# Performance work log

Hardware: AMD Instinct MI355X
Metric: run time of the kernel (lower is better)

The kernel has to match this reference:

```python
import jax, jax.numpy as jnp
import numpy as np

MODEL_DIM = 1024
TOTAL_DIM = 1024
N_HEADS = 16
HEAD_DIM = TOTAL_DIM // N_HEADS


def setup_inputs() -> dict:
    key = jax.random.key(0)
    k1, k2, k3 = jax.random.split(key, 3)
    query = jax.random.normal(k1, (2, 2048, MODEL_DIM), dtype=jnp.float32)
    # nn.Linear(model_dim, 3*total_dim, bias=False): store as [in, out] for x @ W
    W_in = jax.random.normal(k2, (MODEL_DIM, 3 * TOTAL_DIM), dtype=jnp.float32) / np.sqrt(MODEL_DIM)
    W_out = jax.random.normal(k3, (TOTAL_DIM, MODEL_DIM), dtype=jnp.float32) / np.sqrt(TOTAL_DIM)
    return {"query": query, "W_in": W_in, "W_out": W_out}


def reference(query, W_in, W_out):
    B, S, _ = query.shape
    qkv = query @ W_in                      # [B, S, 3*D]
    q, k, v = jnp.split(qkv, 3, axis=-1)    # each [B, S, D]

    def to_heads(t):
        return t.reshape(B, S, N_HEADS, HEAD_DIM).transpose(0, 2, 1, 3)  # [B,H,S,d]

    q, k, v = to_heads(q), to_heads(k), to_heads(v)
    scale = 1.0 / np.sqrt(HEAD_DIM).astype(np.float32)
    scores = jnp.einsum('bhqd,bhkd->bhqk', q, k) * scale  # [B,H,S,S]
    causal = jnp.tril(jnp.ones((S, S), dtype=bool))
    scores = jnp.where(causal, scores, jnp.finfo(scores.dtype).min)
    probs = jax.nn.softmax(scores, axis=-1)
    attn = jnp.einsum('bhqk,bhkd->bhqd', probs, v)        # [B,H,S,d]
    attn = attn.transpose(0, 2, 1, 3).reshape(B, S, TOTAL_DIM)
    return attn @ W_out                     # [B, S, model_dim]
```

## Files before the change

kernel.cpp:

```cpp
#include <hip/hip_runtime.h>


typedef __bf16 bf16x8 __attribute__((ext_vector_type(8)));
typedef float f32x4 __attribute__((ext_vector_type(4)));
typedef int i32x4 __attribute__((ext_vector_type(4)));

#define B_   2
#define S_   2048
#define DM   1024
#define NH   16
#define HD   64
#define N3   3072
#define M_   4096

#define SCALE_LOG2E 0.180336884f

__device__ __forceinline__ unsigned short f2bf(float f) {
  unsigned int u = __float_as_uint(f);
  u += 0x7fffu + ((u >> 16) & 1u);
  return (unsigned short)(u >> 16);
}

__device__ __forceinline__ void gload_lds16(void* lds, const void* g) {
  __builtin_amdgcn_global_load_lds(
      (__attribute__((address_space(1))) void*)g,
      (__attribute__((address_space(3))) void*)lds, 16, 0, 0);
}

__global__ __launch_bounds__(256) void f32_to_bf16_vec(
    const float4* __restrict__ in, unsigned short* __restrict__ out, int n4) {
  int i = blockIdx.x * 256 + threadIdx.x;
  if (i < n4) {
    float4 v = in[i];
    ushort4 o;
    o.x = f2bf(v.x); o.y = f2bf(v.y); o.z = f2bf(v.z); o.w = f2bf(v.w);
    *(ushort4*)(&out[(size_t)i * 4]) = o;
  }
}

__global__ __launch_bounds__(256) void transpose_f32_bf16(
    const float* __restrict__ in, unsigned short* __restrict__ out, int R, int C) {
  __shared__ float tile[32][33];
  const int tx = threadIdx.x, ty = threadIdx.y;
  const int x = blockIdx.x * 32 + tx;
  const int y0 = blockIdx.y * 32;
#pragma unroll
  for (int j = 0; j < 32; j += 8)
    tile[ty + j][tx] = in[(size_t)(y0 + ty + j) * C + x];
  __syncthreads();
  const int ox = y0 + tx;
  const int oy0 = blockIdx.x * 32;
#pragma unroll
  for (int j = 0; j < 32; j += 8)
    out[(size_t)(oy0 + ty + j) * R + ox] = f2bf(tile[tx][ty + j]);
}

__global__ __launch_bounds__(256) void transpose_v(
    const unsigned short* __restrict__ qkv, unsigned short* __restrict__ vT) {
  __shared__ unsigned short tile[32][33];
  const int tx = threadIdx.x, ty = threadIdx.y;
  const int c0 = blockIdx.x * 32;
  const int r0 = blockIdx.y * 32;
#pragma unroll
  for (int j = 0; j < 32; j += 8)
    tile[ty + j][tx] = qkv[(size_t)(r0 + ty + j) * N3 + 2 * DM + c0 + tx];
  __syncthreads();
  const int b = r0 >> 11;
  const int srow = (r0 & 2047);
  const int head = c0 >> 6;
#pragma unroll
  for (int j = 0; j < 32; j += 8) {
    const int d = (c0 & 63) + ty + j;
    vT[(size_t)((b * NH + head) * HD + d) * S_ + srow + tx] = tile[tx][ty + j];
  }
}

template <int OUT_BF16>
__global__ __launch_bounds__(256) void gemm_abt(
    const unsigned short* __restrict__ A, const unsigned short* __restrict__ Bt,
    void* __restrict__ Cv, int M, int N, int K) {
  __shared__ __align__(16) unsigned short a_sm[128 * 32];
  __shared__ __align__(16) unsigned short b_sm[128 * 32];
  const int tid = threadIdx.x;
  const int lane = tid & 63, wave = tid >> 6;
  const int quad = lane >> 4, l15 = lane & 15;
  const int row0 = blockIdx.y * 128, col0 = blockIdx.x * 128;
  const int wm = (wave >> 1) * 64, wn = (wave & 1) * 64;

  f32x4 acc[4][4];
#pragma unroll
  for (int i = 0; i < 4; i++)
#pragma unroll
    for (int j = 0; j < 4; j++) acc[i][j] = (f32x4){0.f, 0.f, 0.f, 0.f};

  const int e0 = tid * 8;

  for (int k0 = 0; k0 < K; k0 += 32) {
    __syncthreads();
#pragma unroll
    for (int i = 0; i < 2; i++) {
      int e = e0 + i * 2048;
      int r = e >> 5, c = e & 31;
      gload_lds16(&a_sm[e], &A[(size_t)(row0 + r) * K + k0 + c]);
      gload_lds16(&b_sm[e], &Bt[(size_t)(col0 + r) * K + k0 + c]);
    }
    __syncthreads();

    bf16x8 af[4], bfb[4];
#pragma unroll
    for (int i = 0; i < 4; i++) {
      af[i]  = *(const bf16x8*)&a_sm[(wm + i * 16 + l15) * 32 + quad * 8];
      bfb[i] = *(const bf16x8*)&b_sm[(wn + i * 16 + l15) * 32 + quad * 8];
    }
#pragma unroll
    for (int i = 0; i < 4; i++)
#pragma unroll
      for (int j = 0; j < 4; j++)
        acc[i][j] = __builtin_amdgcn_mfma_f32_16x16x32_bf16(af[i], bfb[j], acc[i][j], 0, 0, 0);
  }

#pragma unroll
  for (int i = 0; i < 4; i++) {
#pragma unroll
    for (int j = 0; j < 4; j++) {
#pragma unroll
      for (int r = 0; r < 4; r++) {
        const int row = row0 + wm + i * 16 + quad * 4 + r;
        const int col = col0 + wn + j * 16 + l15;
        const float v = acc[i][j][r];
        if (OUT_BF16)
          ((unsigned short*)Cv)[(size_t)row * N + col] = f2bf(v);
        else
          ((float*)Cv)[(size_t)row * N + col] = v;
      }
    }
  }
}

__global__ __launch_bounds__(512, 4) void attn_fused3(
    const unsigned short* __restrict__ qkv,
    const unsigned short* __restrict__ vT,
    unsigned short* __restrict__ attnout) {
  const int h = blockIdx.y, b = blockIdx.z;
  const int qt = (b == 0) ? blockIdx.x : (15 - blockIdx.x);
  const int tid = threadIdx.x;
  const int lane = tid & 63, wave = tid >> 6;
  const int quad = lane >> 4, l15 = lane & 15;
  const int sw = l15 & 7;

  __shared__ __align__(16) unsigned short k_sm[2 * 4096];
  __shared__ __align__(16) unsigned short vt_sm[2 * 4096];

  const int Q0 = qt * 128;
  const int qrow = Q0 + wave * 16 + l15;
  const int wrow0 = Q0 + wave * 16;

  bf16x8 qf[2];
  {
    const unsigned short* qp = qkv + (size_t)(b * S_ + qrow) * N3 + h * HD + quad * 8;
    qf[0] = *(const bf16x8*)qp;
    qf[1] = *(const bf16x8*)(qp + 32);
  }

  f32x4 o[4];
#pragma unroll
  for (int n = 0; n < 4; n++) o[n] = (f32x4){0.f, 0.f, 0.f, 0.f};
  float lsum = 0.f;

  const int r0s = tid >> 3;
  const int gch = ((tid & 7) ^ (r0s & 7)) * 8;
  const unsigned short* kgb = qkv + (size_t)(b * S_ + r0s) * N3 + DM + h * HD + gch;
  const unsigned short* vgb = vT + (size_t)((b * NH + h) * HD + r0s) * S_ + gch;

  const int addrA = (((quad * 2) & 3) * 16 + l15) * 4;
  const int addrB = (((quad * 2 + 1) & 3) * 16 + l15) * 4;

  const int nt = 2 * qt + 2;
  gload_lds16(&k_sm[tid * 8], kgb);
  gload_lds16(&vt_sm[tid * 8], vgb);

  for (int t = 0; t < nt; t++) {
    __syncthreads();
    if (t + 1 < nt) {
      const int nb = ((t + 1) & 1) * 4096;
      gload_lds16(&k_sm[nb + tid * 8], kgb + (size_t)(t + 1) * 64 * N3);
      gload_lds16(&vt_sm[nb + tid * 8], vgb + (t + 1) * 64);
    }
    if (t * 64 > wrow0 + 15) continue;

    const unsigned short* kb = &k_sm[(t & 1) * 4096];
    const unsigned short* vb = &vt_sm[(t & 1) * 4096];

    f32x4 s[4];
#pragma unroll
    for (int mb = 0; mb < 4; mb++) s[mb] = (f32x4){0.f, 0.f, 0.f, 0.f};
#pragma unroll
    for (int mb = 0; mb < 4; mb++) {
      const int ro = (mb * 16 + l15) * 64;
      bf16x8 kf0 = *(const bf16x8*)&kb[ro + ((quad ^ sw) << 3)];
      bf16x8 kf1 = *(const bf16x8*)&kb[ro + (((4 + quad) ^ sw) << 3)];
      s[mb] = __builtin_amdgcn_mfma_f32_16x16x32_bf16(kf0, qf[0], s[mb], 0, 0, 0);
      s[mb] = __builtin_amdgcn_mfma_f32_16x16x32_bf16(kf1, qf[1], s[mb], 0, 0, 0);
    }

    if (t * 64 + 63 <= wrow0) {
#pragma unroll
      for (int mb = 0; mb < 4; mb++)
#pragma unroll
        for (int r = 0; r < 4; r++)
          s[mb][r] = exp2f(s[mb][r] * SCALE_LOG2E);
    } else {
      const int kb0 = t * 64 + quad * 4;
#pragma unroll
      for (int mb = 0; mb < 4; mb++)
#pragma unroll
        for (int r = 0; r < 4; r++) {
          const float e = exp2f(s[mb][r] * SCALE_LOG2E);
          s[mb][r] = (kb0 + mb * 16 + r <= qrow) ? e : 0.f;
        }
    }
#pragma unroll
    for (int mb = 0; mb < 4; mb++)
      lsum += (s[mb][0] + s[mb][1]) + (s[mb][2] + s[mb][3]);

    int pk[4][2];
#pragma unroll
    for (int mb = 0; mb < 4; mb++) {
      const unsigned u0 = __float_as_uint(s[mb][0]) + 0x8000u;
      const unsigned u1 = __float_as_uint(s[mb][1]) + 0x8000u;
      const unsigned u2 = __float_as_uint(s[mb][2]) + 0x8000u;
      const unsigned u3 = __float_as_uint(s[mb][3]) + 0x8000u;
      pk[mb][0] = (int)__builtin_amdgcn_perm(u1, u0, 0x07060302u);
      pk[mb][1] = (int)__builtin_amdgcn_perm(u3, u2, 0x07060302u);
    }

    const bool hi = quad >= 2;
#pragma unroll
    for (int ks = 0; ks < 2; ks++) {
      const int m0 = 2 * ks, m1 = m0 + 1;
      const int f0a = __builtin_amdgcn_ds_bpermute(addrA, pk[m0][0]);
      const int f0b = __builtin_amdgcn_ds_bpermute(addrA, pk[m1][0]);
      const int f1a = __builtin_amdgcn_ds_bpermute(addrA, pk[m0][1]);
      const int f1b = __builtin_amdgcn_ds_bpermute(addrA, pk[m1][1]);
      const int f2a = __builtin_amdgcn_ds_bpermute(addrB, pk[m0][0]);
      const int f2b = __builtin_amdgcn_ds_bpermute(addrB, pk[m1][0]);
      const int f3a = __builtin_amdgcn_ds_bpermute(addrB, pk[m0][1]);
      const int f3b = __builtin_amdgcn_ds_bpermute(addrB, pk[m1][1]);
      i32x4 fr;
      fr.x = hi ? f0b : f0a;
      fr.y = hi ? f1b : f1a;
      fr.z = hi ? f2b : f2a;
      fr.w = hi ? f3b : f3a;
      const bf16x8 pfrag = __builtin_bit_cast(bf16x8, fr);
#pragma unroll
      for (int mb = 0; mb < 4; mb++) {
        const int ro = (mb * 16 + l15) * 64;
        bf16x8 vf = *(const bf16x8*)&vb[ro + (((ks * 4 + quad) ^ sw) << 3)];
        o[mb] = __builtin_amdgcn_mfma_f32_16x16x32_bf16(vf, pfrag, o[mb], 0, 0, 0);
      }
    }
  }

  float l = lsum;
  l += __shfl_xor(l, 16);
  l += __shfl_xor(l, 32);
  const float inv = 1.0f / l;
  const size_t grow = (size_t)(b * S_ + qrow);
#pragma unroll
  for (int mb = 0; mb < 4; mb++) {
    ushort4 w;
    w.x = f2bf(o[mb][0] * inv);
    w.y = f2bf(o[mb][1] * inv);
    w.z = f2bf(o[mb][2] * inv);
    w.w = f2bf(o[mb][3] * inv);
    *(ushort4*)&attnout[grow * DM + h * HD + mb * 16 + quad * 4] = w;
  }
}

extern "C" void kernel_launch(void* const* d_in, const int* in_sizes, int n_in,
                              void* d_out, int out_size, void* d_ws, size_t ws_size,
                              hipStream_t stream) {
  const float* query = (const float*)d_in[0];
  const float* w_in  = (const float*)d_in[1];
  const float* w_out = (const float*)d_in[2];
  float* out = (float*)d_out;

  char* ws = (char*)d_ws;
  unsigned short* qbf     = (unsigned short*)(ws);
  unsigned short* vT      = (unsigned short*)(ws);
  unsigned short* w_in_t  = (unsigned short*)(ws + 8388608);
  unsigned short* w_out_t = (unsigned short*)(ws + 14680064);
  unsigned short* qkv     = (unsigned short*)(ws + 16777216);
  unsigned short* attn    = (unsigned short*)(ws + 41943040);

  f32_to_bf16_vec<<<dim3(M_ * DM / 1024), dim3(256), 0, stream>>>(
      (const float4*)query, qbf, M_ * DM / 4);
  transpose_f32_bf16<<<dim3(N3 / 32, DM / 32), dim3(32, 8), 0, stream>>>(w_in, w_in_t, DM, N3);
  transpose_f32_bf16<<<dim3(DM / 32, DM / 32), dim3(32, 8), 0, stream>>>(w_out, w_out_t, DM, DM);
  gemm_abt<1><<<dim3(N3 / 128, M_ / 128), dim3(256), 0, stream>>>(qbf, w_in_t, qkv, M_, N3, DM);
  transpose_v<<<dim3(DM / 32, M_ / 32), dim3(32, 8), 0, stream>>>(qkv, vT);
  attn_fused3<<<dim3(S_ / 128, NH, B_), dim3(512), 0, stream>>>(qkv, vT, attn);
  gemm_abt<0><<<dim3(DM / 128, M_ / 128), dim3(256), 0, stream>>>(attn, w_out_t, out, M_, DM, DM);
}
```

Measured before the change: 203.6 us.

## Fold softmax scale into W_in and give each wave two query row groups

The softmax scale times log2(e) is now folded into the Q columns of the transposed W_in, which removes a multiply per score in the attention kernel. The attention kernel moves from 8 waves of 16 rows each to 4 waves, each covering two 16-row query groups 64 rows apart. K and V fragments are loaded from LDS into registers once per tile and reused for both groups, which halves LDS fragment traffic per MFMA. The cost is higher register pressure, fewer waves per block, and Q rounded to bf16 after scaling, which changes numerics slightly.

```diff
diff --git a/kernel.cpp b/kernel.cpp
--- a/kernel.cpp
+++ b/kernel.cpp
@@ -39,7 +39,8 @@
 }
 
 __global__ __launch_bounds__(256) void transpose_f32_bf16(
-    const float* __restrict__ in, unsigned short* __restrict__ out, int R, int C) {
+    const float* __restrict__ in, unsigned short* __restrict__ out, int R, int C,
+    int scale_rows, float scale) {
   __shared__ float tile[32][33];
   const int tx = threadIdx.x, ty = threadIdx.y;
   const int x = blockIdx.x * 32 + tx;
@@ -51,8 +52,12 @@
   const int ox = y0 + tx;
   const int oy0 = blockIdx.x * 32;
 #pragma unroll
-  for (int j = 0; j < 32; j += 8)
-    out[(size_t)(oy0 + ty + j) * R + ox] = f2bf(tile[tx][ty + j]);
+  for (int j = 0; j < 32; j += 8) {
+    const int orow = oy0 + ty + j;
+    float v = tile[tx][ty + j];
+    if (orow < scale_rows) v *= scale;
+    out[(size_t)orow * R + ox] = f2bf(v);
+  }
 }
 
 __global__ __launch_bounds__(256) void transpose_v(
@@ -137,7 +142,7 @@
   }
 }
 
-__global__ __launch_bounds__(512, 4) void attn_fused3(
+__global__ __launch_bounds__(256, 2) void attn_fused5(
     const unsigned short* __restrict__ qkv,
     const unsigned short* __restrict__ vT,
     unsigned short* __restrict__ attnout) {
@@ -151,21 +156,26 @@
   __shared__ __align__(16) unsigned short k_sm[2 * 4096];
   __shared__ __align__(16) unsigned short vt_sm[2 * 4096];
 
-  const int Q0 = qt * 128;
-  const int qrow = Q0 + wave * 16 + l15;
-  const int wrow0 = Q0 + wave * 16;
-
-  bf16x8 qf[2];
+  const int wrow0 = qt * 128 + wave * 16;
+  const int qrow0 = wrow0 + l15;
+  const int qrow1 = qrow0 + 64;
+
+  bf16x8 qf[2][2];
   {
-    const unsigned short* qp = qkv + (size_t)(b * S_ + qrow) * N3 + h * HD + quad * 8;
-    qf[0] = *(const bf16x8*)qp;
-    qf[1] = *(const bf16x8*)(qp + 32);
-  }
-
-  f32x4 o[4];
-#pragma unroll
-  for (int n = 0; n < 4; n++) o[n] = (f32x4){0.f, 0.f, 0.f, 0.f};
-  float lsum = 0.f;
+    const unsigned short* qp0 = qkv + (size_t)(b * S_ + qrow0) * N3 + h * HD + quad * 8;
+    qf[0][0] = *(const bf16x8*)qp0;
+    qf[0][1] = *(const bf16x8*)(qp0 + 32);
+    const unsigned short* qp1 = qp0 + (size_t)64 * N3;
+    qf[1][0] = *(const bf16x8*)qp1;
+    qf[1][1] = *(const bf16x8*)(qp1 + 32);
+  }
+
+  f32x4 o[2][4];
+#pragma unroll
+  for (int g = 0; g < 2; g++)
+#pragma unroll
+    for (int n = 0; n < 4; n++) o[g][n] = (f32x4){0.f, 0.f, 0.f, 0.f};
+  float lsum[2] = {0.f, 0.f};
 
   const int r0s = tid >> 3;
   const int gch = ((tid & 7) ^ (r0s & 7)) * 8;
@@ -177,103 +187,130 @@
 
   const int nt = 2 * qt + 2;
   gload_lds16(&k_sm[tid * 8], kgb);
+  gload_lds16(&k_sm[tid * 8 + 2048], kgb + (size_t)32 * N3);
   gload_lds16(&vt_sm[tid * 8], vgb);
+  gload_lds16(&vt_sm[tid * 8 + 2048], vgb + (size_t)32 * S_);
 
   for (int t = 0; t < nt; t++) {
     __syncthreads();
     if (t + 1 < nt) {
       const int nb = ((t + 1) & 1) * 4096;
-      gload_lds16(&k_sm[nb + tid * 8], kgb + (size_t)(t + 1) * 64 * N3);
-      gload_lds16(&vt_sm[nb + tid * 8], vgb + (t + 1) * 64);
-    }
-    if (t * 64 > wrow0 + 15) continue;
+      const unsigned short* kgt = kgb + (size_t)(t + 1) * 64 * N3;
+      const unsigned short* vgt = vgb + (t + 1) * 64;
+      gload_lds16(&k_sm[nb + tid * 8], kgt);
+      gload_lds16(&k_sm[nb + tid * 8 + 2048], kgt + (size_t)32 * N3);
+      gload_lds16(&vt_sm[nb + tid * 8], vgt);
+      gload_lds16(&vt_sm[nb + tid * 8 + 2048], vgt + (size_t)32 * S_);
+    }
 
     const unsigned short* kb = &k_sm[(t & 1) * 4096];
     const unsigned short* vb = &vt_sm[(t & 1) * 4096];
-
-    f32x4 s[4];
-#pragma unroll
-    for (int mb = 0; mb < 4; mb++) s[mb] = (f32x4){0.f, 0.f, 0.f, 0.f};
+    const unsigned short* kb0 = kb + l15 * 64 + ((quad ^ sw) << 3);
+    const unsigned short* kb1 = kb + l15 * 64 + (((4 + quad) ^ sw) << 3);
+    const unsigned short* vb0 = vb + l15 * 64 + ((quad ^ sw) << 3);
+    const unsigned short* vb1 = vb + l15 * 64 + (((4 + quad) ^ sw) << 3);
+
+    bf16x8 kf0[4], kf1[4];
 #pragma unroll
     for (int mb = 0; mb < 4; mb++) {
-      const int ro = (mb * 16 + l15) * 64;
-      bf16x8 kf0 = *(const bf16x8*)&kb[ro + ((quad ^ sw) << 3)];
-      bf16x8 kf1 = *(const bf16x8*)&kb[ro + (((4 + quad) ^ sw) << 3)];
-      s[mb] = __builtin_amdgcn_mfma_f32_16x16x32_bf16(kf0, qf[0], s[mb], 0, 0, 0);
-      s[mb] = __builtin_amdgcn_mfma_f32_16x16x32_bf16(kf1, qf[1], s[mb], 0, 0, 0);
-    }
-
-    if (t * 64 + 63 <= wrow0) {
+      kf0[mb] = *(const bf16x8*)&kb0[mb * 1024];
+      kf1[mb] = *(const bf16x8*)&kb1[mb * 1024];
+    }
+    bf16x8 vf0[4], vf1[4];
+#pragma unroll
+    for (int mb = 0; mb < 4; mb++) {
+      vf0[mb] = *(const bf16x8*)&vb0[mb * 1024];
+      vf1[mb] = *(const bf16x8*)&vb1[mb * 1024];
+    }
+
+#pragma unroll
+    for (int g = 0; g < 2; g++) {
+      if (g == 0 && t + 1 >= nt) continue;
+      const int qr = (g == 0) ? qrow0 : qrow1;
+
+      f32x4 s[4];
+#pragma unroll
+      for (int mb = 0; mb < 4; mb++) s[mb] = (f32x4){0.f, 0.f, 0.f, 0.f};
+#pragma unroll
+      for (int mb = 0; mb < 4; mb++) {
+        s[mb] = __builtin_amdgcn_mfma_f32_16x16x32_bf16(kf0[mb], qf[g][0], s[mb], 0, 0, 0);
+        s[mb] = __builtin_amdgcn_mfma_f32_16x16x32_bf16(kf1[mb], qf[g][1], s[mb], 0, 0, 0);
+      }
+
+      if (t != nt - 2 + g) {
+#pragma unroll
+        for (int mb = 0; mb < 4; mb++)
+#pragma unroll
+          for (int r = 0; r < 4; r++)
+            s[mb][r] = exp2f(s[mb][r]);
+      } else {
+        const int kq0 = t * 64 + quad * 4;
+#pragma unroll
+        for (int mb = 0; mb < 4; mb++)
+#pragma unroll
+          for (int r = 0; r < 4; r++) {
+            const float e = exp2f(s[mb][r]);
+            s[mb][r] = (kq0 + mb * 16 + r <= qr) ? e : 0.f;
+          }
+      }
 #pragma unroll
       for (int mb = 0; mb < 4; mb++)
-#pragma unroll
-        for (int r = 0; r < 4; r++)
-          s[mb][r] = exp2f(s[mb][r] * SCALE_LOG2E);
-    } else {
-      const int kb0 = t * 64 + quad * 4;
-#pragma unroll
-      for (int mb = 0; mb < 4; mb++)
-#pragma unroll
-        for (int r = 0; r < 4; r++) {
-          const float e = exp2f(s[mb][r] * SCALE_LOG2E);
-          s[mb][r] = (kb0 + mb * 16 + r <= qrow) ? e : 0.f;
+        lsum[g] += (s[mb][0] + s[mb][1]) + (s[mb][2] + s[mb][3]);
+
+      int pk[4][2];
+#pragma unroll
+      for (int mb = 0; mb < 4; mb++) {
+        const unsigned u0 = __float_as_uint(s[mb][0]) + 0x8000u;
+        const unsigned u1 = __float_as_uint(s[mb][1]) + 0x8000u;
+        const unsigned u2 = __float_as_uint(s[mb][2]) + 0x8000u;
+        const unsigned u3 = __float_as_uint(s[mb][3]) + 0x8000u;
+        pk[mb][0] = (int)__builtin_amdgcn_perm(u1, u0, 0x07060302u);
+        pk[mb][1] = (int)__builtin_amdgcn_perm(u3, u2, 0x07060302u);
+      }
+
+      const bool hi = quad >= 2;
+#pragma unroll
+      for (int ks = 0; ks < 2; ks++) {
+        const int m0 = 2 * ks, m1 = m0 + 1;
+        const int f0a = __builtin_amdgcn_ds_bpermute(addrA, pk[m0][0]);
+        const int f0b = __builtin_amdgcn_ds_bpermute(addrA, pk[m1][0]);
+        const int f1a = __builtin_amdgcn_ds_bpermute(addrA, pk[m0][1]);
+        const int f1b = __builtin_amdgcn_ds_bpermute(addrA, pk[m1][1]);
+        const int f2a = __builtin_amdgcn_ds_bpermute(addrB, pk[m0][0]);
+        const int f2b = __builtin_amdgcn_ds_bpermute(addrB, pk[m1][0]);
+        const int f3a = __builtin_amdgcn_ds_bpermute(addrB, pk[m0][1]);
+        const int f3b = __builtin_amdgcn_ds_bpermute(addrB, pk[m1][1]);
+        i32x4 fr;
+        fr.x = hi ? f0b : f0a;
+        fr.y = hi ? f1b : f1a;
+        fr.z = hi ? f2b : f2a;
+        fr.w = hi ? f3b : f3a;
+        const bf16x8 pfrag = __builtin_bit_cast(bf16x8, fr);
+#pragma unroll
+        for (int mb = 0; mb < 4; mb++) {
+          const bf16x8 vf = (ks == 0) ? vf0[mb] : vf1[mb];
+          o[g][mb] = __builtin_amdgcn_mfma_f32_16x16x32_bf16(vf, pfrag, o[g][mb], 0, 0, 0);
         }
-    }
-#pragma unroll
-    for (int mb = 0; mb < 4; mb++)
-      lsum += (s[mb][0] + s[mb][1]) + (s[mb][2] + s[mb][3]);
-
-    int pk[4][2];
+      }
+    }
+  }
+
+#pragma unroll
+  for (int g = 0; g < 2; g++) {
+    float l = lsum[g];
+    l += __shfl_xor(l, 16);
+    l += __shfl_xor(l, 32);
+    const float inv = 1.0f / l;
+    const size_t grow = (size_t)(b * S_ + ((g == 0) ? qrow0 : qrow1));
 #pragma unroll
     for (int mb = 0; mb < 4; mb++) {
-      const unsigned u0 = __float_as_uint(s[mb][0]) + 0x8000u;
-      const unsigned u1 = __float_as_uint(s[mb][1]) + 0x8000u;
-      const unsigned u2 = __float_as_uint(s[mb][2]) + 0x8000u;
-      const unsigned u3 = __float_as_uint(s[mb][3]) + 0x8000u;
-      pk[mb][0] = (int)__builtin_amdgcn_perm(u1, u0, 0x07060302u);
-      pk[mb][1] = (int)__builtin_amdgcn_perm(u3, u2, 0x07060302u);
-    }
-
-    const bool hi = quad >= 2;
-#pragma unroll
-    for (int ks = 0; ks < 2; ks++) {
-      const int m0 = 2 * ks, m1 = m0 + 1;
-      const int f0a = __builtin_amdgcn_ds_bpermute(addrA, pk[m0][0]);
-      const int f0b = __builtin_amdgcn_ds_bpermute(addrA, pk[m1][0]);
-      const int f1a = __builtin_amdgcn_ds_bpermute(addrA, pk[m0][1]);
-      const int f1b = __builtin_amdgcn_ds_bpermute(addrA, pk[m1][1]);
-      const int f2a = __builtin_amdgcn_ds_bpermute(addrB, pk[m0][0]);
-      const int f2b = __builtin_amdgcn_ds_bpermute(addrB, pk[m1][0]);
-      const int f3a = __builtin_amdgcn_ds_bpermute(addrB, pk[m0][1]);
-      const int f3b = __builtin_amdgcn_ds_bpermute(addrB, pk[m1][1]);
-      i32x4 fr;
-      fr.x = hi ? f0b : f0a;
-      fr.y = hi ? f1b : f1a;
-      fr.z = hi ? f2b : f2a;
-      fr.w = hi ? f3b : f3a;
-      const bf16x8 pfrag = __builtin_bit_cast(bf16x8, fr);
-#pragma unroll
-      for (int mb = 0; mb < 4; mb++) {
-        const int ro = (mb * 16 + l15) * 64;
-        bf16x8 vf = *(const bf16x8*)&vb[ro + (((ks * 4 + quad) ^ sw) << 3)];
-        o[mb] = __builtin_amdgcn_mfma_f32_16x16x32_bf16(vf, pfrag, o[mb], 0, 0, 0);
-      }
-    }
-  }
-
-  float l = lsum;
-  l += __shfl_xor(l, 16);
-  l += __shfl_xor(l, 32);
-  const float inv = 1.0f / l;
-  const size_t grow = (size_t)(b * S_ + qrow);
-#pragma unroll
-  for (int mb = 0; mb < 4; mb++) {
-    ushort4 w;
-    w.x = f2bf(o[mb][0] * inv);
-    w.y = f2bf(o[mb][1] * inv);
-    w.z = f2bf(o[mb][2] * inv);
-    w.w = f2bf(o[mb][3] * inv);
-    *(ushort4*)&attnout[grow * DM + h * HD + mb * 16 + quad * 4] = w;
+      ushort4 w;
+      w.x = f2bf(o[g][mb][0] * inv);
+      w.y = f2bf(o[g][mb][1] * inv);
+      w.z = f2bf(o[g][mb][2] * inv);
+      w.w = f2bf(o[g][mb][3] * inv);
+      *(ushort4*)&attnout[grow * DM + h * HD + mb * 16 + quad * 4] = w;
+    }
   }
 }
 
@@ -295,10 +332,12 @@
 
   f32_to_bf16_vec<<<dim3(M_ * DM / 1024), dim3(256), 0, stream>>>(
       (const float4*)query, qbf, M_ * DM / 4);
-  transpose_f32_bf16<<<dim3(N3 / 32, DM / 32), dim3(32, 8), 0, stream>>>(w_in, w_in_t, DM, N3);
-  transpose_f32_bf16<<<dim3(DM / 32, DM / 32), dim3(32, 8), 0, stream>>>(w_out, w_out_t, DM, DM);
+  transpose_f32_bf16<<<dim3(N3 / 32, DM / 32), dim3(32, 8), 0, stream>>>(
+      w_in, w_in_t, DM, N3, DM, SCALE_LOG2E);
+  transpose_f32_bf16<<<dim3(DM / 32, DM / 32), dim3(32, 8), 0, stream>>>(
+      w_out, w_out_t, DM, DM, 0, 1.0f);
   gemm_abt<1><<<dim3(N3 / 128, M_ / 128), dim3(256), 0, stream>>>(qbf, w_in_t, qkv, M_, N3, DM);
   transpose_v<<<dim3(DM / 32, M_ / 32), dim3(32, 8), 0, stream>>>(qkv, vT);
-  attn_fused3<<<dim3(S_ / 128, NH, B_), dim3(512), 0, stream>>>(qkv, vT, attn);
+  attn_fused5<<<dim3(16, NH, B_), dim3(256), 0, stream>>>(qkv, vT, attn);
   gemm_abt<0><<<dim3(DM / 128, M_ / 128), dim3(256), 0, stream>>>(attn, w_out_t, out, M_, DM, DM);
 }
```

After: 215.0 us. +5.6%, slower.
